# Optimization experiments

Hardware: AMD Instinct MI355X
Metric: run time of the kernel (lower is better)

The kernel has to match this reference:

```python
import jax, jax.numpy as jnp
import numpy as np

N = 50000      # nodes
E = 1_000_000  # edges (avg degree 20)
D = 64         # hidden dim
L = 3          # num dynamics layers
LN_EPS = 1e-5


def layernorm(h, g, b):
    mu = jnp.mean(h, axis=-1, keepdims=True)
    var = jnp.mean(jnp.square(h - mu), axis=-1, keepdims=True)
    return (h - mu) * jax.lax.rsqrt(var + LN_EPS) * g + b


def transformer_conv(h, src, dst, Wq, bq, Wk, bk, Wv, bv, Ws, bs):
    # PyG TransformerConv, heads=1, concat=False, beta=False, root_weight=True
    n = h.shape[0]
    d = Wq.shape[1]
    q = h @ Wq + bq            # [N, D] queries (dst side)
    k = h @ Wk + bk            # [N, D] keys   (src side)
    v = h @ Wv + bv            # [N, D] values (src side)
    logits = jnp.sum(q[dst] * k[src], axis=-1) / jnp.sqrt(jnp.asarray(d, h.dtype))  # [E]
    # segment softmax over incoming edges of each dst node
    m = jax.ops.segment_max(logits, dst, num_segments=n)      # [N]
    e = jnp.exp(logits - m[dst])                               # [E]
    s = jax.ops.segment_sum(e, dst, num_segments=n)            # [N]
    a = e / s[dst]                                             # [E]
    agg = jax.ops.segment_sum(a[:, None] * v[src], dst, num_segments=n)  # [N, D]
    return agg + h @ Ws + bs   # root/skip connection


def setup_inputs() -> dict:
    key = jax.random.key(0)
    ks = jax.random.split(key, 24)
    w = lambda k, shape: (jax.random.normal(k, shape, jnp.float32) * 0.05)
    inp = {
        "x": jax.random.normal(ks[0], (N, D), jnp.float32),
        "edge_index": jax.random.randint(ks[1], (2, E), 0, N, jnp.int32),
        # input_proj conv params
        "Wq0": w(ks[2], (D, D)), "bq0": w(ks[3], (D,)),
        "Wk0": w(ks[4], (D, D)), "bk0": w(ks[5], (D,)),
        "Wv0": w(ks[6], (D, D)), "bv0": w(ks[7], (D,)),
        "Ws0": w(ks[8], (D, D)), "bs0": w(ks[9], (D,)),
        "ln0_g": jnp.ones((D,), jnp.float32), "ln0_b": jnp.zeros((D,), jnp.float32),
        # stacked dynamics conv params [L, ...]
        "Wq": w(ks[10], (L, D, D)), "bq": w(ks[11], (L, D)),
        "Wk": w(ks[12], (L, D, D)), "bk": w(ks[13], (L, D)),
        "Wv": w(ks[14], (L, D, D)), "bv": w(ks[15], (L, D)),
        "Ws": w(ks[16], (L, D, D)), "bs": w(ks[17], (L, D)),
        "ln_g": jnp.ones((L, D), jnp.float32), "ln_b": jnp.zeros((L, D), jnp.float32),
    }
    return inp


def reference(x, edge_index, Wq0, bq0, Wk0, bk0, Wv0, bv0, Ws0, bs0, ln0_g, ln0_b,
              Wq, bq, Wk, bk, Wv, bv, Ws, bs, ln_g, ln_b):
    src, dst = edge_index[0], edge_index[1]
    h = transformer_conv(x, src, dst, Wq0, bq0, Wk0, bk0, Wv0, bv0, Ws0, bs0)
    h = jax.nn.relu(layernorm(h, ln0_g, ln0_b))
    # dropout is identity in eval mode
    for i in range(L):
        hi = transformer_conv(h, src, dst, Wq[i], bq[i], Wk[i], bk[i],
                              Wv[i], bv[i], Ws[i], bs[i])
        h = jax.nn.relu(layernorm(hi + h, ln_g[i], ln_b[i]))
    return h
```

## Files before the change

### kernel.cpp

```cpp
#include <hip/hip_runtime.h>
#include <math.h>

#define NN 50000
#define NE 1000000
#define CAP 64
#define LN_EPS 1e-5f
#define ROW_TILES 3125
#define GEMM_BLOCKS 782
#define BE_T 250112
#define ELL_BLOCKS 977

typedef __attribute__((ext_vector_type(8))) short short8;
typedef __attribute__((ext_vector_type(8))) unsigned short ushort8;
typedef __attribute__((ext_vector_type(4))) float f32x4;

__device__ __forceinline__ unsigned short f2bf(float f) {
  union { float f; unsigned u; } v; v.f = f;
  unsigned r = v.u + 0x7FFF + ((v.u >> 16) & 1);
  return (unsigned short)(r >> 16);
}
__device__ __forceinline__ float bf2f(unsigned short b) {
  union { unsigned u; float f; } v; v.u = ((unsigned)b) << 16;
  return v.f;
}

__global__ __launch_bounds__(256) void wprep(
    const float* __restrict__ Wq0, const float* __restrict__ bq0,
    const float* __restrict__ Wk0, const float* __restrict__ bk0,
    const float* __restrict__ Wv0, const float* __restrict__ bv0,
    const float* __restrict__ Ws0, const float* __restrict__ bs0,
    const float* __restrict__ WqL, const float* __restrict__ bqL,
    const float* __restrict__ WkL, const float* __restrict__ bkL,
    const float* __restrict__ WvL, const float* __restrict__ bvL,
    const float* __restrict__ WsL, const float* __restrict__ bsL,
    unsigned short* __restrict__ Wt, float* __restrict__ Bc,
    int* __restrict__ cursor) {
  int tid = blockIdx.x * 256 + threadIdx.x;
  if (tid < NN) cursor[tid] = 0;
  if (tid >= 4 * 256 * 64) return;
  int lyr = tid >> 14;
  int rem = tid & 16383;
  int c = rem >> 6;
  int k = rem & 63;
  int m = c >> 6;
  int n = c & 63;
  const float *W, *B;
  if (lyr == 0) {
    const float* Wm[4] = {Wq0, Wk0, Wv0, Ws0};
    const float* Bm[4] = {bq0, bk0, bv0, bs0};
    W = Wm[m]; B = Bm[m];
  } else {
    const float* Wm[4] = {WqL, WkL, WvL, WsL};
    const float* Bm[4] = {bqL, bkL, bvL, bsL};
    W = Wm[m] + (size_t)(lyr - 1) * 4096;
    B = Bm[m] + (size_t)(lyr - 1) * 64;
  }
  Wt[(size_t)lyr * 16384 + (size_t)c * 64 + k] = f2bf(W[(size_t)k * 64 + n]);
  if (k == 0) Bc[lyr * 256 + c] = B[n];
}

__global__ __launch_bounds__(256) void gemm_qkvs(
    const float* __restrict__ h, const unsigned short* __restrict__ Wt,
    const float* __restrict__ Bc, unsigned short* __restrict__ Qb,
    unsigned short* __restrict__ Kb, unsigned short* __restrict__ Vb,
    float* __restrict__ Sf,
    const int* __restrict__ ei, int* __restrict__ cursor,
    unsigned int* __restrict__ ell, int nGemm) {
  __shared__ unsigned short lw[256 * 72];
  int tid = threadIdx.x;

  if ((int)blockIdx.x >= nGemm) {
    int t = (blockIdx.x - nGemm) * 256 + tid;
    int e[4]; bool v[4]; int s[4], d[4], p[4];
#pragma unroll
    for (int i = 0; i < 4; ++i) { e[i] = t + i * BE_T; v[i] = e[i] < NE; }
#pragma unroll
    for (int i = 0; i < 4; ++i) {
      if (v[i]) { s[i] = ei[e[i]]; d[i] = ei[NE + e[i]]; }
    }
#pragma unroll
    for (int i = 0; i < 4; ++i) {
      if (v[i]) p[i] = atomicAdd(&cursor[d[i]], 1);
    }
#pragma unroll
    for (int i = 0; i < 4; ++i) {
      if (v[i] && p[i] < CAP)
        atomicExch(&ell[(size_t)d[i] * CAP + p[i]], (unsigned int)s[i]);
    }
    return;
  }

#pragma unroll
  for (int it = 0; it < 8; ++it) {
    int id = it * 256 + tid;
    int row = id >> 3, cc = id & 7;
    float4 src = *reinterpret_cast<const float4*>(Wt + (size_t)row * 64 + cc * 8);
    *reinterpret_cast<float4*>(lw + (size_t)row * 72 + cc * 8) = src;
  }
  __syncthreads();

  int wave = tid >> 6, lane = tid & 63;
  int tile = blockIdx.x * 4 + wave;
  if (tile >= ROW_TILES) return;
  int lo = lane & 15, hi = lane >> 4;
  int row = tile * 16 + lo;
  const float* hrow = h + (size_t)row * 64;

  auto packA = [&](const float* p) {
    float4 x = *reinterpret_cast<const float4*>(p);
    float4 y = *reinterpret_cast<const float4*>(p + 4);
    short8 r;
    r[0] = (short)f2bf(x.x); r[1] = (short)f2bf(x.y);
    r[2] = (short)f2bf(x.z); r[3] = (short)f2bf(x.w);
    r[4] = (short)f2bf(y.x); r[5] = (short)f2bf(y.y);
    r[6] = (short)f2bf(y.z); r[7] = (short)f2bf(y.w);
    return r;
  };
  short8 a0 = packA(hrow + hi * 8);
  short8 a1 = packA(hrow + 32 + hi * 8);

  int rb = tile * 16 + hi * 4;

  auto mm = [&](int brow, float bias) {
    f32x4 acc = {bias, bias, bias, bias};
    const unsigned short* wr = lw + (size_t)brow * 72 + hi * 8;
    short8 b0 = *reinterpret_cast<const short8*>(wr);
    short8 b1 = *reinterpret_cast<const short8*>(wr + 32);
    acc = __builtin_amdgcn_mfma_f32_16x16x32_bf16(a0, b0, acc, 0, 0, 0);
    acc = __builtin_amdgcn_mfma_f32_16x16x32_bf16(a1, b1, acc, 0, 0, 0);
    return acc;
  };

#pragma unroll
  for (int ct = 0; ct < 4; ++ct) {
    int col = ct * 16 + lo;
    f32x4 acc = mm(col, Bc[col]);
#pragma unroll
    for (int r = 0; r < 4; ++r) Qb[(size_t)(rb + r) * 64 + col] = f2bf(acc[r]);
  }
#pragma unroll
  for (int ct = 0; ct < 4; ++ct) {
    int col = ct * 16 + lo;
    f32x4 acc = mm(64 + col, Bc[64 + col]);
#pragma unroll
    for (int r = 0; r < 4; ++r) Kb[(size_t)(rb + r) * 64 + col] = f2bf(acc[r]);
  }
#pragma unroll
  for (int ct = 0; ct < 4; ++ct) {
    int col = ct * 16 + lo;
    f32x4 acc = mm(128 + col, Bc[128 + col]);
#pragma unroll
    for (int r = 0; r < 4; ++r) Vb[(size_t)(rb + r) * 64 + col] = f2bf(acc[r]);
  }
#pragma unroll
  for (int ct = 0; ct < 4; ++ct) {
    int col = ct * 16 + lo;
    f32x4 acc = mm(192 + col, Bc[192 + col]);
#pragma unroll
    for (int r = 0; r < 4; ++r) Sf[(size_t)(rb + r) * 64 + col] = acc[r];
  }
}

__global__ __launch_bounds__(256) void edge_fused(
    const unsigned short* __restrict__ Qb, const unsigned short* __restrict__ Kb,
    const unsigned short* __restrict__ Vb, const float* __restrict__ Sf,
    const unsigned int* __restrict__ ell, const int* __restrict__ cursor,
    const float* __restrict__ ln_g, const float* __restrict__ ln_b,
    const float* __restrict__ h_res, float* __restrict__ h_out, int use_res) {
  int node = blockIdx.x * 4 + (threadIdx.x >> 6);
  if (node >= NN) return;
  int lane = threadIdx.x & 63;
  int e = lane >> 3, d = lane & 7;

  int deg = cursor[node];
  if (deg > CAP) deg = CAP;
  const unsigned int* lst = ell + (size_t)node * CAP;

  ushort8 q8 = *reinterpret_cast<const ushort8*>(Qb + (size_t)node * 64 + d * 8);
  float q[8];
#pragma unroll
  for (int j = 0; j < 8; ++j) q[j] = bf2f(q8[j]);

  int passes = (deg + 7) >> 3;

  auto ld8 = [&](int p, const unsigned short* T) {
    int slot = p * 8 + e;
    int src = (slot < deg) ? (int)lst[slot] : 0;
    return *reinterpret_cast<const ushort8*>(T + (size_t)src * 64 + d * 8);
  };

  float acc[8] = {0.f, 0.f, 0.f, 0.f, 0.f, 0.f, 0.f, 0.f};
  float ssum = 0.f;
  ushort8 k0 = ld8(0, Kb), v0 = ld8(0, Vb);
  ushort8 k1 = ld8(1, Kb), v1 = ld8(1, Vb);
  for (int p = 0; p < passes; ++p) {
    ushort8 k2 = ld8(p + 2, Kb), v2 = ld8(p + 2, Vb);
    bool valid = (p * 8 + e) < deg;
    float dp = 0.f;
#pragma unroll
    for (int j = 0; j < 8; ++j) dp += q[j] * bf2f(k0[j]);
    dp += __shfl_xor(dp, 1, 64);
    dp += __shfl_xor(dp, 2, 64);
    dp += __shfl_xor(dp, 4, 64);
    float w = valid ? __expf(dp * 0.125f) : 0.f;
    ssum += w;
#pragma unroll
    for (int j = 0; j < 8; ++j) acc[j] = fmaf(w, bf2f(v0[j]), acc[j]);
    k0 = k1; v0 = v1; k1 = k2; v1 = v2;
  }
#pragma unroll
  for (int off = 8; off <= 32; off <<= 1) {
#pragma unroll
    for (int j = 0; j < 8; ++j) acc[j] += __shfl_xor(acc[j], off, 64);
    ssum += __shfl_xor(ssum, off, 64);
  }
  float inv = (ssum > 0.f) ? (1.f / ssum) : 0.f;

  const float* sp = Sf + (size_t)node * 64 + d * 8;
  float o[8];
#pragma unroll
  for (int j = 0; j < 8; ++j) o[j] = acc[j] * inv + sp[j];
  if (use_res) {
    const float* rp = h_res + (size_t)node * 64 + d * 8;
#pragma unroll
    for (int j = 0; j < 8; ++j) o[j] += rp[j];
  }

  float sum = 0.f;
#pragma unroll
  for (int j = 0; j < 8; ++j) sum += o[j];
  sum += __shfl_xor(sum, 1, 64);
  sum += __shfl_xor(sum, 2, 64);
  sum += __shfl_xor(sum, 4, 64);
  float mu = sum * (1.f / 64.f);
  float vs = 0.f;
#pragma unroll
  for (int j = 0; j < 8; ++j) { float t = o[j] - mu; vs += t * t; }
  vs += __shfl_xor(vs, 1, 64);
  vs += __shfl_xor(vs, 2, 64);
  vs += __shfl_xor(vs, 4, 64);
  float rstd = rsqrtf(vs * (1.f / 64.f) + LN_EPS);
  if (e == 0) {
    const float* gp = ln_g + d * 8;
    const float* bp = ln_b + d * 8;
    float y[8];
#pragma unroll
    for (int j = 0; j < 8; ++j)
      y[j] = fmaxf((o[j] - mu) * rstd * gp[j] + bp[j], 0.f);
    float* op = h_out + (size_t)node * 64 + d * 8;
    *reinterpret_cast<float4*>(op) = make_float4(y[0], y[1], y[2], y[3]);
    *reinterpret_cast<float4*>(op + 4) = make_float4(y[4], y[5], y[6], y[7]);
  }
}

extern "C" void kernel_launch(void* const* d_in, const int* in_sizes, int n_in,
                              void* d_out, int out_size, void* d_ws, size_t ws_size,
                              hipStream_t stream) {
  const float* x    = (const float*)d_in[0];
  const int*   ei   = (const int*)d_in[1];
  const float* Wq0  = (const float*)d_in[2];
  const float* bq0  = (const float*)d_in[3];
  const float* Wk0  = (const float*)d_in[4];
  const float* bk0  = (const float*)d_in[5];
  const float* Wv0  = (const float*)d_in[6];
  const float* bv0  = (const float*)d_in[7];
  const float* Ws0  = (const float*)d_in[8];
  const float* bs0  = (const float*)d_in[9];
  const float* ln0g = (const float*)d_in[10];
  const float* ln0b = (const float*)d_in[11];
  const float* WqL  = (const float*)d_in[12];
  const float* bqL  = (const float*)d_in[13];
  const float* WkL  = (const float*)d_in[14];
  const float* bkL  = (const float*)d_in[15];
  const float* WvL  = (const float*)d_in[16];
  const float* bvL  = (const float*)d_in[17];
  const float* WsL  = (const float*)d_in[18];
  const float* bsL  = (const float*)d_in[19];
  const float* lnG  = (const float*)d_in[20];
  const float* lnB  = (const float*)d_in[21];

  float* h = (float*)d_out;

  char* ws = (char*)d_ws;
  size_t off = 0;
  unsigned short* Qb = (unsigned short*)(ws + off);  off += (size_t)NN * 64 * 2;
  unsigned short* Kb = (unsigned short*)(ws + off);  off += (size_t)NN * 64 * 2;
  unsigned short* Vb = (unsigned short*)(ws + off);  off += (size_t)NN * 64 * 2;
  float* Sf = (float*)(ws + off);                    off += (size_t)NN * 64 * 4;
  unsigned int* ell = (unsigned int*)(ws + off);     off += (size_t)NN * CAP * 4;
  int* cursor = (int*)(ws + off);                    off += (size_t)NN * 4;
  unsigned short* Wt = (unsigned short*)(ws + off);  off += (size_t)4 * 256 * 64 * 2;
  float* Bc = (float*)(ws + off);                    off += (size_t)4 * 256 * 4;

  wprep<<<256, 256, 0, stream>>>(Wq0, bq0, Wk0, bk0, Wv0, bv0, Ws0, bs0,
                                 WqL, bqL, WkL, bkL, WvL, bvL, WsL, bsL,
                                 Wt, Bc, cursor);

  for (int layer = 0; layer < 4; ++layer) {
    const float* hin = (layer == 0) ? x : h;
    const float* lg = (layer == 0) ? ln0g : lnG + (size_t)(layer - 1) * 64;
    const float* lb = (layer == 0) ? ln0b : lnB + (size_t)(layer - 1) * 64;
    int extra = (layer == 0) ? ELL_BLOCKS : 0;
    gemm_qkvs<<<GEMM_BLOCKS + extra, 256, 0, stream>>>(
        hin, Wt + (size_t)layer * 16384, Bc + (size_t)layer * 256,
        Qb, Kb, Vb, Sf, ei, cursor, ell, GEMM_BLOCKS);
    edge_fused<<<(NN + 3) / 4, 256, 0, stream>>>(
        Qb, Kb, Vb, Sf, ell, cursor, lg, lb, h, h, layer > 0 ? 1 : 0);
  }
}
```

Before: 424.0 us.

## Partition ELL build per XCD, store 16-bit indices, split QKVS GEMM

Builds the ELL adjacency with blocks grouped by blockIdx&7, assuming that maps to an XCD. Each group owns one range of destination nodes and claims edge chunks through a per-group atomic counter, so cursor atomics and ELL writes stay in one L2. ELL source ids are stored as 16-bit values, which halves the adjacency footprint the edge kernel gathers. The QKVS GEMM now uses twice as many blocks, each loading half the weights into LDS and producing either Q/K or V/S. The cost is that every group re-reads the full dst array, and the 16-bit indices only work because N is below 65536.

```diff
diff --git a/kernel.cpp b/kernel.cpp
--- a/kernel.cpp
+++ b/kernel.cpp
@@ -6,9 +6,10 @@
 #define CAP 64
 #define LN_EPS 1e-5f
 #define ROW_TILES 3125
-#define GEMM_BLOCKS 782
-#define BE_T 250112
+#define GEMM_BLOCKS 1564
 #define ELL_BLOCKS 977
+#define NCHUNK 3907
+#define NPX 6250
 
 typedef __attribute__((ext_vector_type(8))) short short8;
 typedef __attribute__((ext_vector_type(8))) unsigned short ushort8;
@@ -34,9 +35,10 @@
     const float* __restrict__ WvL, const float* __restrict__ bvL,
     const float* __restrict__ WsL, const float* __restrict__ bsL,
     unsigned short* __restrict__ Wt, float* __restrict__ Bc,
-    int* __restrict__ cursor) {
+    int* __restrict__ cursor, int* __restrict__ xcd_work) {
   int tid = blockIdx.x * 256 + threadIdx.x;
   if (tid < NN) cursor[tid] = 0;
+  if (tid < 8) xcd_work[tid] = 0;
   if (tid >= 4 * 256 * 64) return;
   int lyr = tid >> 14;
   int rem = tid & 16383;
@@ -65,42 +67,50 @@
     unsigned short* __restrict__ Kb, unsigned short* __restrict__ Vb,
     float* __restrict__ Sf,
     const int* __restrict__ ei, int* __restrict__ cursor,
-    unsigned int* __restrict__ ell, int nGemm) {
-  __shared__ unsigned short lw[256 * 72];
+    unsigned short* __restrict__ ell, int* __restrict__ xcd_work, int nGemm) {
+  __shared__ unsigned short lw[128 * 72];
   int tid = threadIdx.x;
+  int lane = tid & 63;
 
   if ((int)blockIdx.x >= nGemm) {
-    int t = (blockIdx.x - nGemm) * 256 + tid;
-    int e[4]; bool v[4]; int s[4], d[4], p[4];
-#pragma unroll
-    for (int i = 0; i < 4; ++i) { e[i] = t + i * BE_T; v[i] = e[i] < NE; }
-#pragma unroll
-    for (int i = 0; i < 4; ++i) {
-      if (v[i]) { s[i] = ei[e[i]]; d[i] = ei[NE + e[i]]; }
-    }
-#pragma unroll
-    for (int i = 0; i < 4; ++i) {
-      if (v[i]) p[i] = atomicAdd(&cursor[d[i]], 1);
-    }
-#pragma unroll
-    for (int i = 0; i < 4; ++i) {
-      if (v[i] && p[i] < CAP)
-        atomicExch(&ell[(size_t)d[i] * CAP + p[i]], (unsigned int)s[i]);
+    int vx = blockIdx.x & 7;
+    int base_node = vx * NPX;
+    for (;;) {
+      int c;
+      if (lane == 0) c = atomicAdd(&xcd_work[vx], 1);
+      c = __shfl(c, 0, 64);
+      if (c >= NCHUNK) break;
+      int base = c * 256 + lane;
+#pragma unroll
+      for (int i = 0; i < 4; ++i) {
+        int e = base + i * 64;
+        if (e < NE) {
+          int dd = ei[NE + e];
+          if ((unsigned)(dd - base_node) < (unsigned)NPX) {
+            int ss = ei[e];
+            int pos = atomicAdd(&cursor[dd], 1);
+            if (pos < CAP) ell[(size_t)dd * CAP + pos] = (unsigned short)ss;
+          }
+        }
+      }
     }
     return;
   }
 
-#pragma unroll
-  for (int it = 0; it < 8; ++it) {
+  int half = blockIdx.x & 1;
+  int rbase = half * 128;
+#pragma unroll
+  for (int it = 0; it < 4; ++it) {
     int id = it * 256 + tid;
     int row = id >> 3, cc = id & 7;
-    float4 src = *reinterpret_cast<const float4*>(Wt + (size_t)row * 64 + cc * 8);
+    float4 src = *reinterpret_cast<const float4*>(
+        Wt + (size_t)(rbase + row) * 64 + cc * 8);
     *reinterpret_cast<float4*>(lw + (size_t)row * 72 + cc * 8) = src;
   }
   __syncthreads();
 
-  int wave = tid >> 6, lane = tid & 63;
-  int tile = blockIdx.x * 4 + wave;
+  int wave = tid >> 6;
+  int tile = (blockIdx.x >> 1) * 4 + wave;
   if (tile >= ROW_TILES) return;
   int lo = lane & 15, hi = lane >> 4;
   int row = tile * 16 + lo;
@@ -131,40 +141,43 @@
     return acc;
   };
 
-#pragma unroll
-  for (int ct = 0; ct < 4; ++ct) {
-    int col = ct * 16 + lo;
-    f32x4 acc = mm(col, Bc[col]);
-#pragma unroll
-    for (int r = 0; r < 4; ++r) Qb[(size_t)(rb + r) * 64 + col] = f2bf(acc[r]);
-  }
-#pragma unroll
-  for (int ct = 0; ct < 4; ++ct) {
-    int col = ct * 16 + lo;
-    f32x4 acc = mm(64 + col, Bc[64 + col]);
-#pragma unroll
-    for (int r = 0; r < 4; ++r) Kb[(size_t)(rb + r) * 64 + col] = f2bf(acc[r]);
-  }
-#pragma unroll
-  for (int ct = 0; ct < 4; ++ct) {
-    int col = ct * 16 + lo;
-    f32x4 acc = mm(128 + col, Bc[128 + col]);
-#pragma unroll
-    for (int r = 0; r < 4; ++r) Vb[(size_t)(rb + r) * 64 + col] = f2bf(acc[r]);
-  }
-#pragma unroll
-  for (int ct = 0; ct < 4; ++ct) {
-    int col = ct * 16 + lo;
-    f32x4 acc = mm(192 + col, Bc[192 + col]);
-#pragma unroll
-    for (int r = 0; r < 4; ++r) Sf[(size_t)(rb + r) * 64 + col] = acc[r];
+  if (half == 0) {
+#pragma unroll
+    for (int ct = 0; ct < 4; ++ct) {
+      int col = ct * 16 + lo;
+      f32x4 acc = mm(col, Bc[col]);
+#pragma unroll
+      for (int r = 0; r < 4; ++r) Qb[(size_t)(rb + r) * 64 + col] = f2bf(acc[r]);
+    }
+#pragma unroll
+    for (int ct = 0; ct < 4; ++ct) {
+      int col = ct * 16 + lo;
+      f32x4 acc = mm(64 + col, Bc[64 + col]);
+#pragma unroll
+      for (int r = 0; r < 4; ++r) Kb[(size_t)(rb + r) * 64 + col] = f2bf(acc[r]);
+    }
+  } else {
+#pragma unroll
+    for (int ct = 0; ct < 4; ++ct) {
+      int col = ct * 16 + lo;
+      f32x4 acc = mm(col, Bc[128 + col]);
+#pragma unroll
+      for (int r = 0; r < 4; ++r) Vb[(size_t)(rb + r) * 64 + col] = f2bf(acc[r]);
+    }
+#pragma unroll
+    for (int ct = 0; ct < 4; ++ct) {
+      int col = ct * 16 + lo;
+      f32x4 acc = mm(64 + col, Bc[192 + col]);
+#pragma unroll
+      for (int r = 0; r < 4; ++r) Sf[(size_t)(rb + r) * 64 + col] = acc[r];
+    }
   }
 }
 
 __global__ __launch_bounds__(256) void edge_fused(
     const unsigned short* __restrict__ Qb, const unsigned short* __restrict__ Kb,
     const unsigned short* __restrict__ Vb, const float* __restrict__ Sf,
-    const unsigned int* __restrict__ ell, const int* __restrict__ cursor,
+    const unsigned short* __restrict__ ell, const int* __restrict__ cursor,
     const float* __restrict__ ln_g, const float* __restrict__ ln_b,
     const float* __restrict__ h_res, float* __restrict__ h_out, int use_res) {
   int node = blockIdx.x * 4 + (threadIdx.x >> 6);
@@ -174,7 +187,7 @@
 
   int deg = cursor[node];
   if (deg > CAP) deg = CAP;
-  const unsigned int* lst = ell + (size_t)node * CAP;
+  const unsigned short* lst = ell + (size_t)node * CAP;
 
   ushort8 q8 = *reinterpret_cast<const ushort8*>(Qb + (size_t)node * 64 + d * 8);
   float q[8];
@@ -287,14 +300,15 @@
   unsigned short* Kb = (unsigned short*)(ws + off);  off += (size_t)NN * 64 * 2;
   unsigned short* Vb = (unsigned short*)(ws + off);  off += (size_t)NN * 64 * 2;
   float* Sf = (float*)(ws + off);                    off += (size_t)NN * 64 * 4;
-  unsigned int* ell = (unsigned int*)(ws + off);     off += (size_t)NN * CAP * 4;
+  unsigned short* ell = (unsigned short*)(ws + off); off += (size_t)NN * CAP * 2;
   int* cursor = (int*)(ws + off);                    off += (size_t)NN * 4;
   unsigned short* Wt = (unsigned short*)(ws + off);  off += (size_t)4 * 256 * 64 * 2;
   float* Bc = (float*)(ws + off);                    off += (size_t)4 * 256 * 4;
+  int* xcd_work = (int*)(ws + off);                  off += 64;
 
   wprep<<<256, 256, 0, stream>>>(Wq0, bq0, Wk0, bk0, Wv0, bv0, Ws0, bs0,
                                  WqL, bqL, WkL, bkL, WvL, bvL, WsL, bsL,
-                                 Wt, Bc, cursor);
+                                 Wt, Bc, cursor, xcd_work);
 
   for (int layer = 0; layer < 4; ++layer) {
     const float* hin = (layer == 0) ? x : h;
@@ -303,7 +317,7 @@
     int extra = (layer == 0) ? ELL_BLOCKS : 0;
     gemm_qkvs<<<GEMM_BLOCKS + extra, 256, 0, stream>>>(
         hin, Wt + (size_t)layer * 16384, Bc + (size_t)layer * 256,
-        Qb, Kb, Vb, Sf, ei, cursor, ell, GEMM_BLOCKS);
+        Qb, Kb, Vb, Sf, ei, cursor, ell, xcd_work, GEMM_BLOCKS);
     edge_fused<<<(NN + 3) / 4, 256, 0, stream>>>(
         Qb, Kb, Vb, Sf, ell, cursor, lg, lb, h, h, layer > 0 ? 1 : 0);
   }
```

After: 745.0 us. 1.76x slower.
